# Kernel tuning notes

Measured on AMD Instinct MI355X. Metric: run time of the kernel, lower is better.

## Reference

```python
import jax, jax.numpy as jnp
import numpy as np

N_NODES = 100000
N_EDGES = 600000
D = 128


def setup_inputs() -> dict:
    key = jax.random.key(0)
    k1, k2, k3, k4, k5, k6 = jax.random.split(key, 6)
    feat = jax.random.normal(k1, (N_NODES, D), dtype=jnp.float32)
    src = jax.random.randint(k2, (N_EDGES,), 0, N_NODES, dtype=jnp.int64)
    dst = jax.random.randint(k3, (N_EDGES,), 0, N_NODES, dtype=jnp.int64)
    W_neigh = jax.random.normal(k4, (D, D), dtype=jnp.float32) * (1.0 / np.sqrt(D))
    b_neigh = jax.random.normal(k5, (D,), dtype=jnp.float32) * 0.02
    W_self = jax.random.normal(k6, (D, D), dtype=jnp.float32) * (1.0 / np.sqrt(D))
    return {"feat": feat, "src": src, "dst": dst,
            "W_neigh": W_neigh, "b_neigh": b_neigh, "W_self": W_self}


def reference(feat, src, dst, W_neigh, b_neigh, W_self):
    # DGL GraphConv(norm='none'): sum-aggregate neighbor features, then linear.
    # agg[i] = sum_{(s->i) in E} feat[s]
    agg = jax.ops.segment_sum(feat[src], dst, num_segments=feat.shape[0])  # [N, D]
    neigh_feat = agg @ W_neigh + b_neigh                                   # [N, Dout]
    self_feat = feat @ W_self                                              # [N, Dout]
    return neigh_feat + self_feat
```

## Files before the change

kernel.cpp:

```cpp
#include <hip/hip_runtime.h>

#define DF 128
#define CAP 16
#define GR 64
#define PBLK 256

typedef __attribute__((ext_vector_type(8))) short short8;
typedef __attribute__((ext_vector_type(4))) float v4f;

__device__ __forceinline__ unsigned short f2bf(float x) {
    unsigned u = __float_as_uint(x);
    unsigned r = (u + 0x7FFFu + ((u >> 16) & 1u)) >> 16;
    return (unsigned short)r;
}
__device__ __forceinline__ float bf2f(unsigned short h) {
    return __uint_as_float((unsigned)h << 16);
}
__device__ __forceinline__ unsigned pack2(float a, float b) {
    return (unsigned)f2bf(a) | ((unsigned)f2bf(b) << 16);
}

__global__ __launch_bounds__(256) void prep_kernel(
    const int* __restrict__ idx32, int nE, int* __restrict__ hdr,
    const float* __restrict__ Wn, const float* __restrict__ Ws,
    unsigned short* __restrict__ Bt, int* __restrict__ counts, int cnt_ints)
{
    const int b = blockIdx.x;
    const int t = threadIdx.x;
    if (b == 0) {
        __shared__ int sh;
        if (t == 0) sh = 0;
        __syncthreads();
        int found = 0;
        for (int i = t; i < 2048 && i < nE; i += 256)
            if (idx32[2 * i + 1] != 0) found = 1;
        if (found) sh = 1;
        __syncthreads();
        if (t == 0) { hdr[0] = sh; hdr[1] = 0; }
    } else if (b <= 128) {
        int idx = (b - 1) * 256 + t;
        int n = idx >> 7, k = idx & 127;
        float v = (n < DF) ? Wn[(size_t)k * DF + n] : Ws[(size_t)k * DF + (n - DF)];
        Bt[idx] = f2bf(v);
    } else {
        int off = ((b - 129) * 256 + t) * 4;
        if (off < cnt_ints)
            *reinterpret_cast<int4*>(counts + off) = make_int4(0, 0, 0, 0);
    }
}

__global__ __launch_bounds__(256) void fused_kernel(
    const float* __restrict__ feat, const unsigned short* __restrict__ Bt,
    const float* __restrict__ bias, unsigned short* __restrict__ Ybf,
    float* __restrict__ out, int M,
    const void* __restrict__ src, const void* __restrict__ dst, int nE,
    int* __restrict__ hdr, int* __restrict__ counts, int* __restrict__ buckets,
    int2* __restrict__ ovf)
{
    const int t = threadIdx.x;

    if (blockIdx.x < PBLK) {
        const int is32 = hdr[0];
        const int stride = PBLK * 256;
        if (is32) {
            const int* sp = (const int*)src;
            const int* dp = (const int*)dst;
            for (int e = blockIdx.x * 256 + t; e < nE; e += stride) {
                int s = sp[e], d = dp[e];
                int pos = atomicAdd(&counts[d], 1);
                if (pos < CAP) {
                    buckets[(size_t)d * CAP + pos] = s;
                } else {
                    int oi = atomicAdd(&hdr[1], 1);
                    ovf[oi] = make_int2(s, d);
                }
            }
        } else {
            const long long* sp = (const long long*)src;
            const long long* dp = (const long long*)dst;
            for (int e = blockIdx.x * 256 + t; e < nE; e += stride) {
                int s = (int)sp[e], d = (int)dp[e];
                int pos = atomicAdd(&counts[d], 1);
                if (pos < CAP) {
                    buckets[(size_t)d * CAP + pos] = s;
                } else {
                    int oi = atomicAdd(&hdr[1], 1);
                    ovf[oi] = make_int2(s, d);
                }
            }
        }
        return;
    }

    __shared__ unsigned short As[GR][136];
    __shared__ unsigned short Ys[GR][136];

    const int wave = t >> 6;
    const int lane = t & 63;
    const int nl   = lane & 15;
    const int quad = lane >> 4;
    const int block_row = (blockIdx.x - PBLK) * GR;

    {
        const float* base = feat + (size_t)block_row * DF;
#pragma unroll
        for (int it = 0; it < 8; it++) {
            const int idx = t * 4 + it * 1024;
            const int row = idx >> 7, col = idx & 127;
            float4 v;
            if (block_row + row < M)
                v = *reinterpret_cast<const float4*>(base + idx);
            else
                v = make_float4(0.f, 0.f, 0.f, 0.f);
            uint2 pk;
            pk.x = pack2(v.x, v.y);
            pk.y = pack2(v.z, v.w);
            *reinterpret_cast<uint2*>(&As[row][col]) = pk;
        }
    }

    const int n0 = wave * 64;
    short8 bfrag[4][4];
#pragma unroll
    for (int ct = 0; ct < 4; ct++)
#pragma unroll
        for (int kk = 0; kk < 4; kk++)
            bfrag[ct][kk] = *reinterpret_cast<const short8*>(
                Bt + (size_t)(n0 + ct * 16 + nl) * DF + kk * 32 + quad * 8);

    float bcol[4];
#pragma unroll
    for (int ct = 0; ct < 4; ct++) {
        int n = n0 + ct * 16 + nl;
        bcol[ct] = (n >= DF) ? bias[n - DF] : 0.f;
    }

    __syncthreads();

#pragma unroll
    for (int rt = 0; rt < 4; rt++) {
        short8 afrag[4];
#pragma unroll
        for (int kk = 0; kk < 4; kk++)
            afrag[kk] = *reinterpret_cast<const short8*>(
                &As[rt * 16 + nl][kk * 32 + quad * 8]);
#pragma unroll
        for (int ct = 0; ct < 4; ct++) {
            v4f acc = {0.f, 0.f, 0.f, 0.f};
#pragma unroll
            for (int kk = 0; kk < 4; kk++)
                acc = __builtin_amdgcn_mfma_f32_16x16x32_bf16(
                    afrag[kk], bfrag[ct][kk], acc, 0, 0, 0);
            const int n = n0 + ct * 16 + nl;
            const int lrow = rt * 16 + quad * 4;
            if (n < DF) {
#pragma unroll
                for (int r = 0; r < 4; r++)
                    Ys[lrow + r][n] = f2bf(acc[r]);
            } else {
#pragma unroll
                for (int r = 0; r < 4; r++) {
                    const int grow = block_row + lrow + r;
                    if (grow < M)
                        out[(size_t)grow * DF + (n - DF)] = acc[r] + bcol[ct];
                }
            }
        }
    }

    __syncthreads();

    {
        const int row = t >> 2;
        const int cb  = (t & 3) * 32;
        const int grow = block_row + row;
        if (grow < M) {
            const uint4* srcp = reinterpret_cast<const uint4*>(&Ys[row][cb]);
            uint4* dstp = reinterpret_cast<uint4*>(Ybf + (size_t)grow * DF + cb);
            dstp[0] = srcp[0];
            dstp[1] = srcp[1];
            dstp[2] = srcp[2];
            dstp[3] = srcp[3];
        }
    }
}

__global__ __launch_bounds__(256) void gather_kernel(
    const unsigned short* __restrict__ Ybf,
    const int* __restrict__ counts, const int* __restrict__ buckets,
    const int* __restrict__ hdr, const int2* __restrict__ ovf,
    float* __restrict__ out, int M, int ngroups)
{
    int gid = blockIdx.x * 256 + threadIdx.x;
    int node = gid >> 5;
    int lane = gid & 31;

    if (node < M) {
        int deg_raw = counts[node];
        int deg = min(deg_raw, CAP);
        const int* b = buckets + (size_t)node * CAP;

        float4 acc = make_float4(0.f, 0.f, 0.f, 0.f);
        int e = 0;
        for (; e + 4 <= deg; e += 4) {
            int4 ss = *reinterpret_cast<const int4*>(b + e);
            ushort4 y0 = *reinterpret_cast<const ushort4*>(Ybf + (size_t)ss.x * DF + lane * 4);
            ushort4 y1 = *reinterpret_cast<const ushort4*>(Ybf + (size_t)ss.y * DF + lane * 4);
            ushort4 y2 = *reinterpret_cast<const ushort4*>(Ybf + (size_t)ss.z * DF + lane * 4);
            ushort4 y3 = *reinterpret_cast<const ushort4*>(Ybf + (size_t)ss.w * DF + lane * 4);
            acc.x += (bf2f(y0.x) + bf2f(y1.x)) + (bf2f(y2.x) + bf2f(y3.x));
            acc.y += (bf2f(y0.y) + bf2f(y1.y)) + (bf2f(y2.y) + bf2f(y3.y));
            acc.z += (bf2f(y0.z) + bf2f(y1.z)) + (bf2f(y2.z) + bf2f(y3.z));
            acc.w += (bf2f(y0.w) + bf2f(y1.w)) + (bf2f(y2.w) + bf2f(y3.w));
        }
        for (; e < deg; e++) {
            int s0 = b[e];
            ushort4 y0 = *reinterpret_cast<const ushort4*>(Ybf + (size_t)s0 * DF + lane * 4);
            acc.x += bf2f(y0.x);
            acc.y += bf2f(y0.y);
            acc.z += bf2f(y0.z);
            acc.w += bf2f(y0.w);
        }

        float* op = out + (size_t)node * DF + lane * 4;
        if (deg_raw <= CAP) {
            float4 o = *reinterpret_cast<const float4*>(op);
            o.x += acc.x; o.y += acc.y; o.z += acc.z; o.w += acc.w;
            *reinterpret_cast<float4*>(op) = o;
        } else {
            unsafeAtomicAdd(op + 0, acc.x);
            unsafeAtomicAdd(op + 1, acc.y);
            unsafeAtomicAdd(op + 2, acc.z);
            unsafeAtomicAdd(op + 3, acc.w);
        }
    }

    int n_ovf = hdr[1];
    for (int i = gid >> 5; i < n_ovf; i += ngroups) {
        int2 sd = ovf[i];
        ushort4 y = *reinterpret_cast<const ushort4*>(
            Ybf + (size_t)sd.x * DF + lane * 4);
        float* op = out + (size_t)sd.y * DF + lane * 4;
        unsafeAtomicAdd(op + 0, bf2f(y.x));
        unsafeAtomicAdd(op + 1, bf2f(y.y));
        unsafeAtomicAdd(op + 2, bf2f(y.z));
        unsafeAtomicAdd(op + 3, bf2f(y.w));
    }
}

extern "C" void kernel_launch(void* const* d_in, const int* in_sizes, int n_in,
                              void* d_out, int out_size, void* d_ws, size_t ws_size,
                              hipStream_t stream) {
    const float* feat = (const float*)d_in[0];
    const void*  src  = d_in[1];
    const void*  dst  = d_in[2];
    const float* Wn   = (const float*)d_in[3];
    const float* bias = (const float*)d_in[4];
    const float* Wsf  = (const float*)d_in[5];
    float* out = (float*)d_out;

    const int M  = in_sizes[0] / DF;
    const int nE = in_sizes[1];

    const size_t cnt_off   = 256;
    const size_t cnt_bytes = (((size_t)(M + 1) * 4) + 255) & ~(size_t)255;
    const size_t bkt_off   = cnt_off + cnt_bytes;
    const size_t bkt_bytes = (size_t)M * CAP * sizeof(int);
    const size_t bt_off    = (bkt_off + bkt_bytes + 255) & ~(size_t)255;
    const size_t bt_bytes  = (size_t)256 * DF * sizeof(unsigned short);
    const size_t y_off     = bt_off + bt_bytes;
    const size_t y_bytes   = (size_t)M * DF * sizeof(unsigned short);
    const size_t ovf_off   = (y_off + y_bytes + 255) & ~(size_t)255;

    int*            hdr     = (int*)d_ws;
    int*            counts  = (int*)((char*)d_ws + cnt_off);
    int*            buckets = (int*)((char*)d_ws + bkt_off);
    unsigned short* Bt      = (unsigned short*)((char*)d_ws + bt_off);
    unsigned short* Ybf     = (unsigned short*)((char*)d_ws + y_off);
    int2*           ovf     = (int2*)((char*)d_ws + ovf_off);

    const int cnt_ints = (int)(cnt_bytes / 4);
    const int nzb = (cnt_ints + 1023) / 1024;
    prep_kernel<<<1 + 128 + nzb, 256, 0, stream>>>(
        (const int*)src, nE, hdr, Wn, Wsf, Bt, counts, cnt_ints);

    const int gemm_blocks = (M + GR - 1) / GR;
    fused_kernel<<<PBLK + gemm_blocks, 256, 0, stream>>>(
        feat, Bt, bias, Ybf, out, M, src, dst, nE,
        hdr, counts, buckets, ovf);

    const int gablocks = (int)(((long long)M * 32 + 255) / 256);
    const int ngroups = gablocks * 8;
    gather_kernel<<<gablocks, 256, 0, stream>>>(
        Ybf, counts, buckets, hdr, ovf, out, M, ngroups);
}
```

Baseline: 193.2 us.

## Interleave edge bucketing into GEMM blocks and widen gather loads to 16B

The fused kernel no longer reserves separate blocks for edge bucketing. Every GEMM block first scatters a contiguous slice of edges into the per-node buckets and then runs its GEMM tile, spreading the atomic work across all blocks. The gather kernel now uses 16 lanes per node with 16-byte loads of 8 bf16 values, and issues all neighbor loads before accumulating to raise memory-level parallelism. Because the GEMM blocks now stall on atomic edge processing first, the two phases are serialized within each block.

```diff
diff --git a/kernel.cpp b/kernel.cpp
--- a/kernel.cpp
+++ b/kernel.cpp
@@ -3,7 +3,6 @@
 #define DF 128
 #define CAP 16
 #define GR 64
-#define PBLK 256
 
 typedef __attribute__((ext_vector_type(8))) short short8;
 typedef __attribute__((ext_vector_type(4))) float v4f;
@@ -57,15 +56,18 @@
     int* __restrict__ hdr, int* __restrict__ counts, int* __restrict__ buckets,
     int2* __restrict__ ovf)
 {
-    const int t = threadIdx.x;
-
-    if (blockIdx.x < PBLK) {
+    const int t   = threadIdx.x;
+    const int bid = blockIdx.x;
+    const int nb  = (int)gridDim.x;
+
+    {
+        const int e0 = (int)((long long)bid * nE / nb);
+        const int e1 = (int)((long long)(bid + 1) * nE / nb);
         const int is32 = hdr[0];
-        const int stride = PBLK * 256;
         if (is32) {
             const int* sp = (const int*)src;
             const int* dp = (const int*)dst;
-            for (int e = blockIdx.x * 256 + t; e < nE; e += stride) {
+            for (int e = e0 + t; e < e1; e += 256) {
                 int s = sp[e], d = dp[e];
                 int pos = atomicAdd(&counts[d], 1);
                 if (pos < CAP) {
@@ -78,7 +80,7 @@
         } else {
             const long long* sp = (const long long*)src;
             const long long* dp = (const long long*)dst;
-            for (int e = blockIdx.x * 256 + t; e < nE; e += stride) {
+            for (int e = e0 + t; e < e1; e += 256) {
                 int s = (int)sp[e], d = (int)dp[e];
                 int pos = atomicAdd(&counts[d], 1);
                 if (pos < CAP) {
@@ -89,7 +91,6 @@
                 }
             }
         }
-        return;
     }
 
     __shared__ unsigned short As[GR][136];
@@ -99,7 +100,7 @@
     const int lane = t & 63;
     const int nl   = lane & 15;
     const int quad = lane >> 4;
-    const int block_row = (blockIdx.x - PBLK) * GR;
+    const int block_row = bid * GR;
 
     {
         const float* base = feat + (size_t)block_row * DF;
@@ -191,61 +192,106 @@
     const int* __restrict__ hdr, const int2* __restrict__ ovf,
     float* __restrict__ out, int M, int ngroups)
 {
-    int gid = blockIdx.x * 256 + threadIdx.x;
-    int node = gid >> 5;
-    int lane = gid & 31;
-
-    if (node < M) {
-        int deg_raw = counts[node];
-        int deg = min(deg_raw, CAP);
+    const int gid  = blockIdx.x * 256 + threadIdx.x;
+    const int grp  = gid >> 4;
+    const int lane = gid & 15;
+    const size_t lo = (size_t)lane * 8;
+
+#define LDY(s) (*reinterpret_cast<const uint4*>(Ybf + (size_t)(s) * DF + lo))
+#define ACC8(Y) do { \
+        a0 += bf2f((unsigned short)((Y).x)); a1 += bf2f((unsigned short)((Y).x >> 16)); \
+        a2 += bf2f((unsigned short)((Y).y)); a3 += bf2f((unsigned short)((Y).y >> 16)); \
+        a4 += bf2f((unsigned short)((Y).z)); a5 += bf2f((unsigned short)((Y).z >> 16)); \
+        a6 += bf2f((unsigned short)((Y).w)); a7 += bf2f((unsigned short)((Y).w >> 16)); \
+    } while (0)
+
+    if (grp < M) {
+        const int node = grp;
+        const int deg_raw = counts[node];
+        const int deg = min(deg_raw, CAP);
         const int* b = buckets + (size_t)node * CAP;
 
-        float4 acc = make_float4(0.f, 0.f, 0.f, 0.f);
-        int e = 0;
-        for (; e + 4 <= deg; e += 4) {
-            int4 ss = *reinterpret_cast<const int4*>(b + e);
-            ushort4 y0 = *reinterpret_cast<const ushort4*>(Ybf + (size_t)ss.x * DF + lane * 4);
-            ushort4 y1 = *reinterpret_cast<const ushort4*>(Ybf + (size_t)ss.y * DF + lane * 4);
-            ushort4 y2 = *reinterpret_cast<const ushort4*>(Ybf + (size_t)ss.z * DF + lane * 4);
-            ushort4 y3 = *reinterpret_cast<const ushort4*>(Ybf + (size_t)ss.w * DF + lane * 4);
-            acc.x += (bf2f(y0.x) + bf2f(y1.x)) + (bf2f(y2.x) + bf2f(y3.x));
-            acc.y += (bf2f(y0.y) + bf2f(y1.y)) + (bf2f(y2.y) + bf2f(y3.y));
-            acc.z += (bf2f(y0.z) + bf2f(y1.z)) + (bf2f(y2.z) + bf2f(y3.z));
-            acc.w += (bf2f(y0.w) + bf2f(y1.w)) + (bf2f(y2.w) + bf2f(y3.w));
-        }
-        for (; e < deg; e++) {
-            int s0 = b[e];
-            ushort4 y0 = *reinterpret_cast<const ushort4*>(Ybf + (size_t)s0 * DF + lane * 4);
-            acc.x += bf2f(y0.x);
-            acc.y += bf2f(y0.y);
-            acc.z += bf2f(y0.z);
-            acc.w += bf2f(y0.w);
-        }
-
-        float* op = out + (size_t)node * DF + lane * 4;
+        float a0 = 0.f, a1 = 0.f, a2 = 0.f, a3 = 0.f;
+        float a4 = 0.f, a5 = 0.f, a6 = 0.f, a7 = 0.f;
+
+        int4 sa = *reinterpret_cast<const int4*>(b);
+        int4 sb = *reinterpret_cast<const int4*>(b + 4);
+        uint4 y0, y1, y2, y3, y4, y5, y6, y7;
+        if (0 < deg) y0 = LDY(sa.x);
+        if (1 < deg) y1 = LDY(sa.y);
+        if (2 < deg) y2 = LDY(sa.z);
+        if (3 < deg) y3 = LDY(sa.w);
+        if (4 < deg) y4 = LDY(sb.x);
+        if (5 < deg) y5 = LDY(sb.y);
+        if (6 < deg) y6 = LDY(sb.z);
+        if (7 < deg) y7 = LDY(sb.w);
+        if (0 < deg) ACC8(y0);
+        if (1 < deg) ACC8(y1);
+        if (2 < deg) ACC8(y2);
+        if (3 < deg) ACC8(y3);
+        if (4 < deg) ACC8(y4);
+        if (5 < deg) ACC8(y5);
+        if (6 < deg) ACC8(y6);
+        if (7 < deg) ACC8(y7);
+
+        if (deg > 8) {
+            int4 sc = *reinterpret_cast<const int4*>(b + 8);
+            int4 sd = *reinterpret_cast<const int4*>(b + 12);
+            uint4 z0, z1, z2, z3, z4, z5, z6, z7;
+            if ( 8 < deg) z0 = LDY(sc.x);
+            if ( 9 < deg) z1 = LDY(sc.y);
+            if (10 < deg) z2 = LDY(sc.z);
+            if (11 < deg) z3 = LDY(sc.w);
+            if (12 < deg) z4 = LDY(sd.x);
+            if (13 < deg) z5 = LDY(sd.y);
+            if (14 < deg) z6 = LDY(sd.z);
+            if (15 < deg) z7 = LDY(sd.w);
+            if ( 8 < deg) ACC8(z0);
+            if ( 9 < deg) ACC8(z1);
+            if (10 < deg) ACC8(z2);
+            if (11 < deg) ACC8(z3);
+            if (12 < deg) ACC8(z4);
+            if (13 < deg) ACC8(z5);
+            if (14 < deg) ACC8(z6);
+            if (15 < deg) ACC8(z7);
+        }
+
+        float* op = out + (size_t)node * DF + lo;
         if (deg_raw <= CAP) {
-            float4 o = *reinterpret_cast<const float4*>(op);
-            o.x += acc.x; o.y += acc.y; o.z += acc.z; o.w += acc.w;
-            *reinterpret_cast<float4*>(op) = o;
+            float4 o0 = *reinterpret_cast<const float4*>(op);
+            float4 o1 = *reinterpret_cast<const float4*>(op + 4);
+            o0.x += a0; o0.y += a1; o0.z += a2; o0.w += a3;
+            o1.x += a4; o1.y += a5; o1.z += a6; o1.w += a7;
+            *reinterpret_cast<float4*>(op)     = o0;
+            *reinterpret_cast<float4*>(op + 4) = o1;
         } else {
-            unsafeAtomicAdd(op + 0, acc.x);
-            unsafeAtomicAdd(op + 1, acc.y);
-            unsafeAtomicAdd(op + 2, acc.z);
-            unsafeAtomicAdd(op + 3, acc.w);
+            unsafeAtomicAdd(op + 0, a0);
+            unsafeAtomicAdd(op + 1, a1);
+            unsafeAtomicAdd(op + 2, a2);
+            unsafeAtomicAdd(op + 3, a3);
+            unsafeAtomicAdd(op + 4, a4);
+            unsafeAtomicAdd(op + 5, a5);
+            unsafeAtomicAdd(op + 6, a6);
+            unsafeAtomicAdd(op + 7, a7);
         }
     }
 
     int n_ovf = hdr[1];
-    for (int i = gid >> 5; i < n_ovf; i += ngroups) {
+    for (int i = grp; i < n_ovf; i += ngroups) {
         int2 sd = ovf[i];
-        ushort4 y = *reinterpret_cast<const ushort4*>(
-            Ybf + (size_t)sd.x * DF + lane * 4);
-        float* op = out + (size_t)sd.y * DF + lane * 4;
-        unsafeAtomicAdd(op + 0, bf2f(y.x));
-        unsafeAtomicAdd(op + 1, bf2f(y.y));
-        unsafeAtomicAdd(op + 2, bf2f(y.z));
-        unsafeAtomicAdd(op + 3, bf2f(y.w));
-    }
+        uint4 y = LDY(sd.x);
+        float* p = out + (size_t)sd.y * DF + lo;
+        unsafeAtomicAdd(p + 0, bf2f((unsigned short)(y.x)));
+        unsafeAtomicAdd(p + 1, bf2f((unsigned short)(y.x >> 16)));
+        unsafeAtomicAdd(p + 2, bf2f((unsigned short)(y.y)));
+        unsafeAtomicAdd(p + 3, bf2f((unsigned short)(y.y >> 16)));
+        unsafeAtomicAdd(p + 4, bf2f((unsigned short)(y.z)));
+        unsafeAtomicAdd(p + 5, bf2f((unsigned short)(y.z >> 16)));
+        unsafeAtomicAdd(p + 6, bf2f((unsigned short)(y.w)));
+        unsafeAtomicAdd(p + 7, bf2f((unsigned short)(y.w >> 16)));
+    }
+#undef LDY
+#undef ACC8
 }
 
 extern "C" void kernel_launch(void* const* d_in, const int* in_sizes, int n_in,
@@ -285,12 +331,12 @@
         (const int*)src, nE, hdr, Wn, Wsf, Bt, counts, cnt_ints);
 
     const int gemm_blocks = (M + GR - 1) / GR;
-    fused_kernel<<<PBLK + gemm_blocks, 256, 0, stream>>>(
+    fused_kernel<<<gemm_blocks, 256, 0, stream>>>(
         feat, Bt, bias, Ybf, out, M, src, dst, nE,
         hdr, counts, buckets, ovf);
 
-    const int gablocks = (int)(((long long)M * 32 + 255) / 256);
-    const int ngroups = gablocks * 8;
+    const int gablocks = (int)(((long long)M * 16 + 255) / 256);
+    const int ngroups  = gablocks * 16;
     gather_kernel<<<gablocks, 256, 0, stream>>>(
         Ybf, counts, buckets, hdr, ovf, out, M, ngroups);
 }
```

Result: slower. 204.5 us (+5.8%).
